# Kernel optimization log

Hardware: AMD Instinct MI355X
Metric: run time of the kernel (lower is better)

Reference implementation:

```python
import jax, jax.numpy as jnp
import numpy as np

N_NODES = 100_000
N_EDGES = 1_600_000
N_FEAT = 64
E_FEAT = 32
OUT_FEAT = 64


def _xavier_normal(key, shape, gain):
    fan_out, fan_in = shape
    std = gain * np.sqrt(2.0 / (fan_in + fan_out))
    return jax.random.normal(key, shape, dtype=jnp.float32) * std


def setup_inputs() -> dict:
    key = jax.random.key(0)
    ks = jax.random.split(key, 9)
    d_cat = 2 * N_FEAT + E_FEAT  # 160
    n_feat = jax.random.normal(ks[0], (N_NODES, N_FEAT), dtype=jnp.float32)
    e_feat = jax.random.normal(ks[1], (N_EDGES, E_FEAT), dtype=jnp.float32)
    src = jax.random.randint(ks[2], (N_EDGES,), 0, N_NODES, dtype=jnp.int32)
    dst = jax.random.randint(ks[3], (N_EDGES,), 0, N_NODES, dtype=jnp.int32)
    gain = np.sqrt(2.0)
    bound_msg = 1.0 / np.sqrt(d_cat)
    return {
        "n_feat": n_feat,
        "e_feat": e_feat,
        "src": src,
        "dst": dst,
        # W_msg uses default torch Linear init (kaiming-uniform-ish); exact init irrelevant for correctness
        "W_msg_w": jax.random.uniform(ks[4], (OUT_FEAT, d_cat), jnp.float32, -bound_msg, bound_msg),
        "W_msg_b": jax.random.uniform(ks[5], (OUT_FEAT,), jnp.float32, -bound_msg, bound_msg),
        # W uses xavier_normal with gain sqrt(2)
        "W_w": _xavier_normal(ks[6], (2 * OUT_FEAT, d_cat), gain),
        "W_b": jax.random.uniform(ks[7], (2 * OUT_FEAT,), jnp.float32, -bound_msg, bound_msg),
        "a": _xavier_normal(ks[8], (2 * OUT_FEAT, 1), gain),
    }


def reference(n_feat, e_feat, src, dst, W_msg_w, W_msg_b, W_w, W_b, a):
    # gather: per-edge concat [E, 2*n_feat + e_feat]
    feat_cat = jnp.concatenate([n_feat[src], n_feat[dst], e_feat], axis=1)
    # edge attention logits: leaky_relu((feat_cat @ W^T + b) @ a)  -> [E]
    w_feat = feat_cat @ W_w.T + W_b                      # [E, 2*out_feat]
    logits = jax.nn.leaky_relu(w_feat @ a[:, 0])         # [E]
    # edge softmax grouped by destination node
    seg_max = jax.ops.segment_max(logits, dst, num_segments=N_NODES)  # [N]
    ex = jnp.exp(logits - seg_max[dst])                  # [E]
    seg_sum = jax.ops.segment_sum(ex, dst, num_segments=N_NODES)     # [N]
    att = ex / seg_sum[dst]                              # [E]
    # messages and weighted scatter-sum aggregation
    msg = feat_cat @ W_msg_w.T + W_msg_b                 # [E, out_feat]
    agg = jax.ops.segment_sum(att[:, None] * msg, dst, num_segments=N_NODES)  # [N, out_feat]
    return jax.nn.relu(agg)
```

## Files before the change

kernel.cpp:

```cpp
#include <hip/hip_runtime.h>
#include <hip/hip_bf16.h>
#include <hip/hip_fp16.h>

#define N_NODES 100000
#define N_EDGES 1600000
#define NF 64
#define EF 32

#define SCAN_B 512
#define SCAN_NB ((N_NODES + SCAN_B - 1) / SCAN_B)


__device__ __forceinline__ unsigned pkh2(float a, float b) {
  __half2 h = __floats2half2_rn(a, b);
  return *reinterpret_cast<unsigned*>(&h);
}

__global__ __launch_bounds__(256) void k0_prep(
    const float* __restrict__ Ww, const float* __restrict__ Wb,
    const float* __restrict__ a, const float* __restrict__ Wmsg,
    float* __restrict__ v, float* __restrict__ W1T, float* __restrict__ W2T,
    float* __restrict__ WmeT) {
  int t = threadIdx.x;
  for (int j = t; j < 160; j += 256) {
    float s = 0.f;
    for (int k = 0; k < 128; ++k) s = fmaf(a[k], Ww[k * 160 + j], s);
    v[j] = s;
  }
  if (t == 0) {
    float s = 0.f;
    for (int k = 0; k < 128; ++k) s = fmaf(a[k], Wb[k], s);
    v[160] = s;
  }
  for (int idx = t; idx < 64 * 64; idx += 256) {
    int j = idx >> 6, i = idx & 63;
    W1T[idx] = Wmsg[i * 160 + j];
    W2T[idx] = Wmsg[i * 160 + 64 + j];
  }
  for (int idx = t; idx < 32 * 64; idx += 256) {
    int j = idx >> 6, i = idx & 63;
    WmeT[idx] = Wmsg[i * 160 + 128 + j];
  }
}

__global__ __launch_bounds__(256) void k1_node(
    const float* __restrict__ nf_g, const float* __restrict__ v,
    const float* __restrict__ W1T, const float* __restrict__ W2T,
    float* __restrict__ s1, float* __restrict__ s2,
    __half* __restrict__ m_src_h, float* __restrict__ m_dst) {
  int n = blockIdx.x * 256 + threadIdx.x;
  if (n >= N_NODES) return;
  const float4* nf4 = (const float4*)(nf_g + (size_t)n * NF);
  float acc[64];
#pragma unroll
  for (int i = 0; i < 64; ++i) acc[i] = 0.f;
  float s1a = 0.f, s2a = 0.f;
  for (int j4 = 0; j4 < 16; ++j4) {
    float4 q = nf4[j4];
    float xs[4] = {q.x, q.y, q.z, q.w};
#pragma unroll
    for (int u = 0; u < 4; ++u) {
      int j = j4 * 4 + u;
      float x = xs[u];
      s1a = fmaf(v[j], x, s1a);
      s2a = fmaf(v[64 + j], x, s2a);
      const float* w = W1T + j * 64;
#pragma unroll
      for (int i = 0; i < 64; ++i) acc[i] = fmaf(w[i], x, acc[i]);
    }
  }
  s1[n] = s1a;
  s2[n] = s2a;
  uint4* ms4 = (uint4*)(m_src_h + (size_t)n * NF);
#pragma unroll
  for (int b = 0; b < 8; ++b)
    ms4[b] = make_uint4(pkh2(acc[b * 8 + 0], acc[b * 8 + 1]),
                        pkh2(acc[b * 8 + 2], acc[b * 8 + 3]),
                        pkh2(acc[b * 8 + 4], acc[b * 8 + 5]),
                        pkh2(acc[b * 8 + 6], acc[b * 8 + 7]));
#pragma unroll
  for (int i = 0; i < 64; ++i) acc[i] = 0.f;
  for (int j4 = 0; j4 < 16; ++j4) {
    float4 q = nf4[j4];
    float xs[4] = {q.x, q.y, q.z, q.w};
#pragma unroll
    for (int u = 0; u < 4; ++u) {
      int j = j4 * 4 + u;
      float x = xs[u];
      const float* w = W2T + j * 64;
#pragma unroll
      for (int i = 0; i < 64; ++i) acc[i] = fmaf(w[i], x, acc[i]);
    }
  }
  float* md = m_dst + (size_t)n * NF;
#pragma unroll
  for (int i = 0; i < 64; ++i) md[i] = acc[i];
}

__global__ __launch_bounds__(256) void k_count(const int* __restrict__ dst,
                                               int* __restrict__ cnt) {
  int e = blockIdx.x * 256 + threadIdx.x;
  if (e < N_EDGES) atomicAdd(&cnt[dst[e]], 1);
}

__global__ __launch_bounds__(SCAN_B) void kS1(const int* __restrict__ cnt,
                                              int* __restrict__ bsum) {
  __shared__ int sh[SCAN_B];
  int t = threadIdx.x;
  int i = blockIdx.x * SCAN_B + t;
  sh[t] = (i < N_NODES) ? cnt[i] : 0;
  __syncthreads();
  for (int d = SCAN_B / 2; d > 0; d >>= 1) {
    if (t < d) sh[t] += sh[t + d];
    __syncthreads();
  }
  if (t == 0) bsum[blockIdx.x] = sh[0];
}

__global__ __launch_bounds__(256) void kS2(const int* __restrict__ bsum,
                                           int* __restrict__ boff,
                                           int* __restrict__ row_ptr) {
  __shared__ int sh[256];
  int t = threadIdx.x;
  sh[t] = (t < SCAN_NB) ? bsum[t] : 0;
  __syncthreads();
  for (int d = 1; d < 256; d <<= 1) {
    int val = (t >= d) ? sh[t - d] : 0;
    __syncthreads();
    sh[t] += val;
    __syncthreads();
  }
  if (t < SCAN_NB) boff[t] = (t == 0) ? 0 : sh[t - 1];
  if (t == 255) row_ptr[N_NODES] = sh[255];
}

__global__ __launch_bounds__(SCAN_B) void kS3(const int* __restrict__ cnt,
                                              const int* __restrict__ boff,
                                              int* __restrict__ row_ptr,
                                              int* __restrict__ cursor) {
  __shared__ int sh[SCAN_B];
  int t = threadIdx.x;
  int i = blockIdx.x * SCAN_B + t;
  int val = (i < N_NODES) ? cnt[i] : 0;
  sh[t] = val;
  __syncthreads();
  for (int d = 1; d < SCAN_B; d <<= 1) {
    int u = (t >= d) ? sh[t - d] : 0;
    __syncthreads();
    sh[t] += u;
    __syncthreads();
  }
  if (i < N_NODES) {
    int excl = boff[blockIdx.x] + sh[t] - val;
    row_ptr[i] = excl;
    cursor[i] = excl;
  }
}

__global__ __launch_bounds__(256) void kE_scatter(
    const int* __restrict__ src, const int* __restrict__ dst,
    const float* __restrict__ e_feat, int* __restrict__ cursor,
    uint4* __restrict__ ef_s4) {
  int e = blockIdx.x * 256 + threadIdx.x;
  if (e >= N_EDGES) return;
  unsigned sn = (unsigned)src[e];
  int dn = dst[e];
  int p = atomicAdd(&cursor[dn], 1);
  const float4* efr = (const float4*)(e_feat + (size_t)e * EF);
  float4 q[8];
#pragma unroll
  for (int i = 0; i < 8; ++i) q[i] = efr[i];
  unsigned u[16];
#pragma unroll
  for (int i = 0; i < 8; ++i) {
    u[2 * i] = pkh2(q[i].x, q[i].y);
    u[2 * i + 1] = pkh2(q[i].z, q[i].w);
  }
#pragma unroll
  for (int j = 0; j < 16; ++j)
    u[j] = (u[j] & ~1u) | ((sn >> j) & 1u);
  u[0] = (u[0] & ~0x10000u) | (((sn >> 16) & 1u) << 16);
  uint4* o = ef_s4 + (size_t)p * 4;
  o[0] = make_uint4(u[0], u[1], u[2], u[3]);
  o[1] = make_uint4(u[4], u[5], u[6], u[7]);
  o[2] = make_uint4(u[8], u[9], u[10], u[11]);
  o[3] = make_uint4(u[12], u[13], u[14], u[15]);
}

__global__ __launch_bounds__(256) void k3_agg(
    const int* __restrict__ row_ptr, const unsigned* __restrict__ efu,
    const __half* __restrict__ m_src_h, const float* __restrict__ s1,
    const float* __restrict__ s2, const float* __restrict__ v,
    const float* __restrict__ m_dst, const float* __restrict__ WmeT,
    const float* __restrict__ Wmsg_b, float* __restrict__ out) {
  int lane = threadIdx.x & 63;
  int wid = threadIdx.x >> 6;
  int n = blockIdx.x * 4 + wid;
  if (n >= N_NODES) return;
  int start = row_ptr[n];
  int end = row_ptr[n + 1];
  int g = lane >> 4;
  int c2 = lane & 15;
  float vlo = v[128 + 2 * c2];
  float vhi = v[128 + 2 * c2 + 1];
  float cbias = v[160];
  float s2n = s2[n];
  float sum_ex = 0.f, acc_ms = 0.f;
  float aefx = 0.f, aefy = 0.f;
  int slot0 = start + g;
  unsigned ucur = efu[(size_t)min(slot0, N_EDGES - 1) * 16 + c2];
  for (int k = start; k < end; k += 4) {
    int slotn = k + 4 + g;
    unsigned unext = efu[(size_t)min(slotn, N_EDGES - 1) * 16 + c2];
    unsigned long long b0 = __ballot((int)(ucur & 1u));
    unsigned long long b1 = __ballot((int)(ucur & 0x10000u));
    int s0 = (int)((b0 >> 0) & 0xFFFF) | ((int)((b1 >> 0) & 1) << 16);
    int s1i = (int)((b0 >> 16) & 0xFFFF) | ((int)((b1 >> 16) & 1) << 16);
    int s2i = (int)((b0 >> 32) & 0xFFFF) | ((int)((b1 >> 32) & 1) << 16);
    int s3 = (int)((b0 >> 48) & 0xFFFF) | ((int)((b1 >> 48) & 1) << 16);
    s0 = min(s0, N_NODES - 1);
    s1i = min(s1i, N_NODES - 1);
    s2i = min(s2i, N_NODES - 1);
    s3 = min(s3, N_NODES - 1);
    int sg = (g < 2) ? (g ? s1i : s0) : ((g == 2) ? s2i : s3);
    float ms0 = __half2float(m_src_h[(size_t)s0 * NF + lane]);
    float ms1 = __half2float(m_src_h[(size_t)s1i * NF + lane]);
    float ms2 = __half2float(m_src_h[(size_t)s2i * NF + lane]);
    float ms3 = __half2float(m_src_h[(size_t)s3 * NF + lane]);
    __half2 h2 = *reinterpret_cast<__half2*>(&ucur);
    float2 ef2 = __half22float2(h2);
    float pt = fmaf(ef2.y, vhi, ef2.x * vlo);
    pt += __shfl_xor(pt, 1);
    pt += __shfl_xor(pt, 2);
    pt += __shfl_xor(pt, 4);
    pt += __shfl_xor(pt, 8);
    float lg = s1[sg] + s2n + pt + cbias;
    float l = lg > 0.f ? lg : 0.01f * lg;
    float ex = __expf(l);
    float exv = ((k + g) < end) ? ex : 0.f;
    aefx = fmaf(exv, ef2.x, aefx);
    aefy = fmaf(exv, ef2.y, aefy);
    float ex0 = __shfl(exv, 0);
    float ex1 = __shfl(exv, 16);
    float ex2 = __shfl(exv, 32);
    float ex3 = __shfl(exv, 48);
    sum_ex += (ex0 + ex1) + (ex2 + ex3);
    acc_ms = fmaf(ex0, ms0, acc_ms);
    acc_ms = fmaf(ex1, ms1, acc_ms);
    acc_ms = fmaf(ex2, ms2, acc_ms);
    acc_ms = fmaf(ex3, ms3, acc_ms);
    ucur = unext;
  }
  aefx += __shfl_xor(aefx, 16);
  aefx += __shfl_xor(aefx, 32);
  aefy += __shfl_xor(aefy, 16);
  aefy += __shfl_xor(aefy, 32);
  float mm = 0.f;
#pragma unroll
  for (int jp = 0; jp < 16; ++jp) {
    float ea = __shfl(aefx, jp);
    float eb = __shfl(aefy, jp);
    mm = fmaf(WmeT[(2 * jp) * 64 + lane], ea, mm);
    mm = fmaf(WmeT[(2 * jp + 1) * 64 + lane], eb, mm);
  }
  float o = 0.f;
  if (sum_ex > 0.f) {
    o = (acc_ms + mm) / sum_ex + m_dst[(size_t)n * NF + lane] + Wmsg_b[lane];
    o = fmaxf(o, 0.f);
  }
  out[(size_t)n * NF + lane] = o;
}

extern "C" void kernel_launch(void* const* d_in, const int* in_sizes, int n_in,
                              void* d_out, int out_size, void* d_ws,
                              size_t ws_size, hipStream_t stream) {
  const float* n_feat = (const float*)d_in[0];
  const float* e_feat = (const float*)d_in[1];
  const int* src = (const int*)d_in[2];
  const int* dst = (const int*)d_in[3];
  const float* Wmsg_w = (const float*)d_in[4];
  const float* Wmsg_b = (const float*)d_in[5];
  const float* W_w = (const float*)d_in[6];
  const float* W_b = (const float*)d_in[7];
  const float* a = (const float*)d_in[8];
  float* out = (float*)d_out;

  char* ws = (char*)d_ws;
  size_t off = 0;
  auto alloc = [&](size_t bytes) -> char* {
    char* p = ws + off;
    off = (off + bytes + 255) & ~(size_t)255;
    return p;
  };
  float* v = (float*)alloc(161 * 4);
  float* W1T = (float*)alloc(64 * 64 * 4);
  float* W2T = (float*)alloc(64 * 64 * 4);
  float* WmeT = (float*)alloc(32 * 64 * 4);
  float* s1 = (float*)alloc(N_NODES * 4);
  float* s2 = (float*)alloc(N_NODES * 4);
  __half* m_src_h = (__half*)alloc((size_t)N_NODES * NF * 2);
  float* m_dst = (float*)alloc((size_t)N_NODES * NF * 4);
  int* cnt = (int*)alloc(N_NODES * 4);
  int* row_ptr = (int*)alloc((N_NODES + 1) * 4);
  int* cursor = (int*)alloc(N_NODES * 4);
  int* bsum = (int*)alloc(SCAN_NB * 4);
  int* boff = (int*)alloc(SCAN_NB * 4);
  __half* ef_s = (__half*)alloc(((size_t)N_EDGES + 8) * EF * 2);
  if (off > ws_size) return;

  k0_prep<<<1, 256, 0, stream>>>(W_w, W_b, a, Wmsg_w, v, W1T, W2T, WmeT);
  k1_node<<<(N_NODES + 255) / 256, 256, 0, stream>>>(n_feat, v, W1T, W2T, s1,
                                                     s2, m_src_h, m_dst);
  hipMemsetAsync(cnt, 0, N_NODES * 4, stream);
  k_count<<<(N_EDGES + 255) / 256, 256, 0, stream>>>(dst, cnt);
  kS1<<<SCAN_NB, SCAN_B, 0, stream>>>(cnt, bsum);
  kS2<<<1, 256, 0, stream>>>(bsum, boff, row_ptr);
  kS3<<<SCAN_NB, SCAN_B, 0, stream>>>(cnt, boff, row_ptr, cursor);
  kE_scatter<<<(N_EDGES + 255) / 256, 256, 0, stream>>>(
      src, dst, e_feat, cursor, (uint4*)ef_s);
  k3_agg<<<(N_NODES + 3) / 4, 256, 0, stream>>>(
      row_ptr, (const unsigned*)ef_s, m_src_h, s1, s2, v, m_dst, WmeT,
      Wmsg_b, out);
}
```

Measured before the change: 609.8 us.

## Merge prep/count and scan/node kernels, record edge ranks, deepen gather prefetch

Fuses the weight prep into the edge-count kernel and the first scan pass into the node-transform kernel using block-index partitioning, which cuts launches and lets independent work share a launch. The count atomic now returns each edge's rank, so the scatter computes its position as row_ptr plus rank instead of doing a second atomic on a cursor array. In the aggregation loop, source indices, the s1 value and m_src gathers are loaded one iteration ahead with a two-deep edge prefetch, to hide gather latency. In exchange it adds a 6.4 MB rank buffer and raises register pressure, and the node kernel's block size grows to 512 threads, which may reduce occupancy for its register-heavy accumulator.

```diff
diff --git a/kernel.cpp b/kernel.cpp
--- a/kernel.cpp
+++ b/kernel.cpp
@@ -9,6 +9,8 @@
 
 #define SCAN_B 512
 #define SCAN_NB ((N_NODES + SCAN_B - 1) / SCAN_B)
+#define CNT_NB ((N_EDGES + 255) / 256)
+#define K1_NB ((N_NODES + 511) / 512)
 
 
 __device__ __forceinline__ unsigned pkh2(float a, float b) {
@@ -16,12 +18,19 @@
   return *reinterpret_cast<unsigned*>(&h);
 }
 
-__global__ __launch_bounds__(256) void k0_prep(
+__global__ __launch_bounds__(256) void kA_count_prep(
+    const int* __restrict__ dst, int* __restrict__ cnt, int* __restrict__ rank,
     const float* __restrict__ Ww, const float* __restrict__ Wb,
     const float* __restrict__ a, const float* __restrict__ Wmsg,
     float* __restrict__ v, float* __restrict__ W1T, float* __restrict__ W2T,
     float* __restrict__ WmeT) {
+  int b = blockIdx.x;
   int t = threadIdx.x;
+  if (b < CNT_NB) {
+    int e = b * 256 + t;
+    if (e < N_EDGES) rank[e] = atomicAdd(&cnt[dst[e]], 1);
+    return;
+  }
   for (int j = t; j < 160; j += 256) {
     float s = 0.f;
     for (int k = 0; k < 128; ++k) s = fmaf(a[k], Ww[k * 160 + j], s);
@@ -43,12 +52,26 @@
   }
 }
 
-__global__ __launch_bounds__(256) void k1_node(
+__global__ __launch_bounds__(512) void kB_scan1_node(
+    const int* __restrict__ cnt, int* __restrict__ bsum,
     const float* __restrict__ nf_g, const float* __restrict__ v,
     const float* __restrict__ W1T, const float* __restrict__ W2T,
     float* __restrict__ s1, float* __restrict__ s2,
     __half* __restrict__ m_src_h, float* __restrict__ m_dst) {
-  int n = blockIdx.x * 256 + threadIdx.x;
+  __shared__ int sh[SCAN_B];
+  int t = threadIdx.x;
+  if (blockIdx.x < SCAN_NB) {
+    int i = blockIdx.x * SCAN_B + t;
+    sh[t] = (i < N_NODES) ? cnt[i] : 0;
+    __syncthreads();
+    for (int d = SCAN_B / 2; d > 0; d >>= 1) {
+      if (t < d) sh[t] += sh[t + d];
+      __syncthreads();
+    }
+    if (t == 0) bsum[blockIdx.x] = sh[0];
+    return;
+  }
+  int n = (blockIdx.x - SCAN_NB) * 512 + t;
   if (n >= N_NODES) return;
   const float4* nf4 = (const float4*)(nf_g + (size_t)n * NF);
   float acc[64];
@@ -95,26 +118,6 @@
   float* md = m_dst + (size_t)n * NF;
 #pragma unroll
   for (int i = 0; i < 64; ++i) md[i] = acc[i];
-}
-
-__global__ __launch_bounds__(256) void k_count(const int* __restrict__ dst,
-                                               int* __restrict__ cnt) {
-  int e = blockIdx.x * 256 + threadIdx.x;
-  if (e < N_EDGES) atomicAdd(&cnt[dst[e]], 1);
-}
-
-__global__ __launch_bounds__(SCAN_B) void kS1(const int* __restrict__ cnt,
-                                              int* __restrict__ bsum) {
-  __shared__ int sh[SCAN_B];
-  int t = threadIdx.x;
-  int i = blockIdx.x * SCAN_B + t;
-  sh[t] = (i < N_NODES) ? cnt[i] : 0;
-  __syncthreads();
-  for (int d = SCAN_B / 2; d > 0; d >>= 1) {
-    if (t < d) sh[t] += sh[t + d];
-    __syncthreads();
-  }
-  if (t == 0) bsum[blockIdx.x] = sh[0];
 }
 
 __global__ __launch_bounds__(256) void kS2(const int* __restrict__ bsum,
@@ -136,8 +139,7 @@
 
 __global__ __launch_bounds__(SCAN_B) void kS3(const int* __restrict__ cnt,
                                               const int* __restrict__ boff,
-                                              int* __restrict__ row_ptr,
-                                              int* __restrict__ cursor) {
+                                              int* __restrict__ row_ptr) {
   __shared__ int sh[SCAN_B];
   int t = threadIdx.x;
   int i = blockIdx.x * SCAN_B + t;
@@ -150,26 +152,23 @@
     sh[t] += u;
     __syncthreads();
   }
-  if (i < N_NODES) {
-    int excl = boff[blockIdx.x] + sh[t] - val;
-    row_ptr[i] = excl;
-    cursor[i] = excl;
-  }
+  if (i < N_NODES) row_ptr[i] = boff[blockIdx.x] + sh[t] - val;
 }
 
 __global__ __launch_bounds__(256) void kE_scatter(
     const int* __restrict__ src, const int* __restrict__ dst,
-    const float* __restrict__ e_feat, int* __restrict__ cursor,
-    uint4* __restrict__ ef_s4) {
+    const int* __restrict__ rank, const int* __restrict__ row_ptr,
+    const float* __restrict__ e_feat, uint4* __restrict__ ef_s4) {
   int e = blockIdx.x * 256 + threadIdx.x;
   if (e >= N_EDGES) return;
   unsigned sn = (unsigned)src[e];
   int dn = dst[e];
-  int p = atomicAdd(&cursor[dn], 1);
+  int rk = rank[e];
   const float4* efr = (const float4*)(e_feat + (size_t)e * EF);
   float4 q[8];
 #pragma unroll
   for (int i = 0; i < 8; ++i) q[i] = efr[i];
+  int p = row_ptr[dn] + rk;
   unsigned u[16];
 #pragma unroll
   for (int i = 0; i < 8; ++i) {
@@ -207,49 +206,69 @@
   float s2n = s2[n];
   float sum_ex = 0.f, acc_ms = 0.f;
   float aefx = 0.f, aefy = 0.f;
-  int slot0 = start + g;
-  unsigned ucur = efu[(size_t)min(slot0, N_EDGES - 1) * 16 + c2];
-  for (int k = start; k < end; k += 4) {
-    int slotn = k + 4 + g;
-    unsigned unext = efu[(size_t)min(slotn, N_EDGES - 1) * 16 + c2];
+  if (start < end) {
+    unsigned ucur = efu[(size_t)min(start + g, N_EDGES - 1) * 16 + c2];
+    unsigned unxt = efu[(size_t)min(start + 4 + g, N_EDGES - 1) * 16 + c2];
     unsigned long long b0 = __ballot((int)(ucur & 1u));
     unsigned long long b1 = __ballot((int)(ucur & 0x10000u));
-    int s0 = (int)((b0 >> 0) & 0xFFFF) | ((int)((b1 >> 0) & 1) << 16);
-    int s1i = (int)((b0 >> 16) & 0xFFFF) | ((int)((b1 >> 16) & 1) << 16);
-    int s2i = (int)((b0 >> 32) & 0xFFFF) | ((int)((b1 >> 32) & 1) << 16);
-    int s3 = (int)((b0 >> 48) & 0xFFFF) | ((int)((b1 >> 48) & 1) << 16);
-    s0 = min(s0, N_NODES - 1);
-    s1i = min(s1i, N_NODES - 1);
-    s2i = min(s2i, N_NODES - 1);
-    s3 = min(s3, N_NODES - 1);
-    int sg = (g < 2) ? (g ? s1i : s0) : ((g == 2) ? s2i : s3);
-    float ms0 = __half2float(m_src_h[(size_t)s0 * NF + lane]);
-    float ms1 = __half2float(m_src_h[(size_t)s1i * NF + lane]);
-    float ms2 = __half2float(m_src_h[(size_t)s2i * NF + lane]);
-    float ms3 = __half2float(m_src_h[(size_t)s3 * NF + lane]);
-    __half2 h2 = *reinterpret_cast<__half2*>(&ucur);
-    float2 ef2 = __half22float2(h2);
-    float pt = fmaf(ef2.y, vhi, ef2.x * vlo);
-    pt += __shfl_xor(pt, 1);
-    pt += __shfl_xor(pt, 2);
-    pt += __shfl_xor(pt, 4);
-    pt += __shfl_xor(pt, 8);
-    float lg = s1[sg] + s2n + pt + cbias;
-    float l = lg > 0.f ? lg : 0.01f * lg;
-    float ex = __expf(l);
-    float exv = ((k + g) < end) ? ex : 0.f;
-    aefx = fmaf(exv, ef2.x, aefx);
-    aefy = fmaf(exv, ef2.y, aefy);
-    float ex0 = __shfl(exv, 0);
-    float ex1 = __shfl(exv, 16);
-    float ex2 = __shfl(exv, 32);
-    float ex3 = __shfl(exv, 48);
-    sum_ex += (ex0 + ex1) + (ex2 + ex3);
-    acc_ms = fmaf(ex0, ms0, acc_ms);
-    acc_ms = fmaf(ex1, ms1, acc_ms);
-    acc_ms = fmaf(ex2, ms2, acc_ms);
-    acc_ms = fmaf(ex3, ms3, acc_ms);
-    ucur = unext;
+    int a0 = min((int)((b0 >> 0) & 0xFFFF) | ((int)((b1 >> 0) & 1) << 16),
+                 N_NODES - 1);
+    int a1 = min((int)((b0 >> 16) & 0xFFFF) | ((int)((b1 >> 16) & 1) << 16),
+                 N_NODES - 1);
+    int a2 = min((int)((b0 >> 32) & 0xFFFF) | ((int)((b1 >> 32) & 1) << 16),
+                 N_NODES - 1);
+    int a3 = min((int)((b0 >> 48) & 0xFFFF) | ((int)((b1 >> 48) & 1) << 16),
+                 N_NODES - 1);
+    int sgA = (g < 2) ? (g ? a1 : a0) : ((g == 2) ? a2 : a3);
+    float s1A = s1[sgA];
+    __half hA0 = m_src_h[(size_t)a0 * NF + lane];
+    __half hA1 = m_src_h[(size_t)a1 * NF + lane];
+    __half hA2 = m_src_h[(size_t)a2 * NF + lane];
+    __half hA3 = m_src_h[(size_t)a3 * NF + lane];
+    for (int k = start; k < end; k += 4) {
+      unsigned ufar = efu[(size_t)min(k + 8 + g, N_EDGES - 1) * 16 + c2];
+      unsigned long long c0 = __ballot((int)(unxt & 1u));
+      unsigned long long c1 = __ballot((int)(unxt & 0x10000u));
+      int e0 = min((int)((c0 >> 0) & 0xFFFF) | ((int)((c1 >> 0) & 1) << 16),
+                   N_NODES - 1);
+      int e1 = min((int)((c0 >> 16) & 0xFFFF) | ((int)((c1 >> 16) & 1) << 16),
+                   N_NODES - 1);
+      int e2 = min((int)((c0 >> 32) & 0xFFFF) | ((int)((c1 >> 32) & 1) << 16),
+                   N_NODES - 1);
+      int e3 = min((int)((c0 >> 48) & 0xFFFF) | ((int)((c1 >> 48) & 1) << 16),
+                   N_NODES - 1);
+      int sgB = (g < 2) ? (g ? e1 : e0) : ((g == 2) ? e2 : e3);
+      float s1B = s1[sgB];
+      __half hB0 = m_src_h[(size_t)e0 * NF + lane];
+      __half hB1 = m_src_h[(size_t)e1 * NF + lane];
+      __half hB2 = m_src_h[(size_t)e2 * NF + lane];
+      __half hB3 = m_src_h[(size_t)e3 * NF + lane];
+      __half2 h2 = *reinterpret_cast<__half2*>(&ucur);
+      float2 ef2 = __half22float2(h2);
+      float pt = fmaf(ef2.y, vhi, ef2.x * vlo);
+      pt += __shfl_xor(pt, 1);
+      pt += __shfl_xor(pt, 2);
+      pt += __shfl_xor(pt, 4);
+      pt += __shfl_xor(pt, 8);
+      float lg = s1A + s2n + pt + cbias;
+      float l = lg > 0.f ? lg : 0.01f * lg;
+      float exv = ((k + g) < end) ? __expf(l) : 0.f;
+      aefx = fmaf(exv, ef2.x, aefx);
+      aefy = fmaf(exv, ef2.y, aefy);
+      float ex0 = __shfl(exv, 0);
+      float ex1 = __shfl(exv, 16);
+      float ex2 = __shfl(exv, 32);
+      float ex3 = __shfl(exv, 48);
+      sum_ex += (ex0 + ex1) + (ex2 + ex3);
+      acc_ms = fmaf(ex0, __half2float(hA0), acc_ms);
+      acc_ms = fmaf(ex1, __half2float(hA1), acc_ms);
+      acc_ms = fmaf(ex2, __half2float(hA2), acc_ms);
+      acc_ms = fmaf(ex3, __half2float(hA3), acc_ms);
+      ucur = unxt;
+      unxt = ufar;
+      hA0 = hB0; hA1 = hB1; hA2 = hB2; hA3 = hB3;
+      s1A = s1B;
+    }
   }
   aefx += __shfl_xor(aefx, 16);
   aefx += __shfl_xor(aefx, 32);
@@ -302,22 +321,21 @@
   float* m_dst = (float*)alloc((size_t)N_NODES * NF * 4);
   int* cnt = (int*)alloc(N_NODES * 4);
   int* row_ptr = (int*)alloc((N_NODES + 1) * 4);
-  int* cursor = (int*)alloc(N_NODES * 4);
+  int* rank = (int*)alloc((size_t)N_EDGES * 4);
   int* bsum = (int*)alloc(SCAN_NB * 4);
   int* boff = (int*)alloc(SCAN_NB * 4);
   __half* ef_s = (__half*)alloc(((size_t)N_EDGES + 8) * EF * 2);
   if (off > ws_size) return;
 
-  k0_prep<<<1, 256, 0, stream>>>(W_w, W_b, a, Wmsg_w, v, W1T, W2T, WmeT);
-  k1_node<<<(N_NODES + 255) / 256, 256, 0, stream>>>(n_feat, v, W1T, W2T, s1,
-                                                     s2, m_src_h, m_dst);
   hipMemsetAsync(cnt, 0, N_NODES * 4, stream);
-  k_count<<<(N_EDGES + 255) / 256, 256, 0, stream>>>(dst, cnt);
-  kS1<<<SCAN_NB, SCAN_B, 0, stream>>>(cnt, bsum);
+  kA_count_prep<<<CNT_NB + 1, 256, 0, stream>>>(dst, cnt, rank, W_w, W_b, a,
+                                                Wmsg_w, v, W1T, W2T, WmeT);
+  kB_scan1_node<<<SCAN_NB + K1_NB, 512, 0, stream>>>(
+      cnt, bsum, n_feat, v, W1T, W2T, s1, s2, m_src_h, m_dst);
   kS2<<<1, 256, 0, stream>>>(bsum, boff, row_ptr);
-  kS3<<<SCAN_NB, SCAN_B, 0, stream>>>(cnt, boff, row_ptr, cursor);
+  kS3<<<SCAN_NB, SCAN_B, 0, stream>>>(cnt, boff, row_ptr);
   kE_scatter<<<(N_EDGES + 255) / 256, 256, 0, stream>>>(
-      src, dst, e_feat, cursor, (uint4*)ef_s);
+      src, dst, rank, row_ptr, e_feat, (uint4*)ef_s);
   k3_agg<<<(N_NODES + 3) / 4, 256, 0, stream>>>(
       row_ptr, (const unsigned*)ef_s, m_src_h, s1, s2, v, m_dst, WmeT,
       Wmsg_b, out);
```

New measurement: 584.8 us. -4.1%, faster.
